# Kernel tuning notes

Measured on AMD Instinct MI355X. Metric: run time of the kernel, lower is better.

## Reference

```python
import jax, jax.numpy as jnp
import numpy as np

TEMP = 0.05
EPS = 1e-6


def _l2norm(x):
    return x / jnp.linalg.norm(x, axis=1, keepdims=True)


def setup_inputs() -> dict:
    key = jax.random.key(0)
    k1, k2, k3, k4 = jax.random.split(key, 4)
    B, D = 4096, 768
    return {
        "feat": jax.random.normal(k1, (B, D), dtype=jnp.float32),
        "feat_gen": jax.random.normal(k2, (B, D), dtype=jnp.float32),
        "feat_aug": jax.random.normal(k3, (B, D), dtype=jnp.float32),
        "targets": jax.random.randint(k4, (B,), 0, 100, dtype=jnp.int64),
    }


def reference(feat, feat_gen, feat_aug, targets):
    B = feat.shape[0]
    on = _l2norm(feat)
    gn = _l2norm(feat_gen)
    an = _l2norm(feat_aug)
    # [B, B] exp-similarity matrices
    exp_ori = jnp.exp(on @ on.T / TEMP)
    exp_gen = jnp.exp(on @ gn.T / TEMP)
    exp_aug = jnp.exp(on @ an.T / TEMP)

    same = (targets[:, None] == targets[None, :])  # [B, B] bool, includes diagonal
    same_f = same.astype(exp_ori.dtype)

    # ---- co loss: anchors vs ori+aug columns ----
    oa = exp_ori + exp_aug
    diff_sum_oa = oa.sum(axis=1) - (oa * same_f).sum(axis=1)        # [B]
    denom_co = diff_sum_oa + exp_gen.sum(axis=1) + EPS              # [B]
    term_o = -jnp.log(exp_ori / (exp_ori + denom_co[:, None]) + EPS)
    term_a = -jnp.log(exp_aug / (exp_aug + denom_co[:, None]) + EPS)
    co_loss = ((term_o + term_a) * same_f).sum() / B

    # ---- ad loss: anchors vs gen columns ----
    diff_sum_g = exp_gen.sum(axis=1) - (exp_gen * same_f).sum(axis=1)
    denom_ad = diff_sum_g + exp_aug.sum(axis=1) + exp_ori.sum(axis=1) + EPS
    term_g = -jnp.log(exp_gen / (exp_gen + denom_ad[:, None]) + EPS)
    ad_loss = (term_g * same_f).sum() / B

    return (ad_loss, co_loss)
```

## Files before the change

kernel.cpp:

```cpp
#include <hip/hip_runtime.h>
#include <hip/hip_bf16.h>
#include <math.h>

#define Bn 4096
#define Dd 768
#define SC2 28.85390081777927f
#define EPSF 1e-6f
#define DG 4.8516519541e8f

#define O_S      0
#define O_SMOA   12288
#define O_SMG    16384
#define ZERO_F   20480
#define O_P      20480
#define O_RM     20608
#define LIST_OFF   262144
#define LCAP       (1u << 19)
#define NB_OFF     33554432

typedef __attribute__((ext_vector_type(8))) short sh8;
typedef __attribute__((ext_vector_type(4))) float f32x4;

#define AS1 __attribute__((address_space(1)))
#define AS3 __attribute__((address_space(3)))

static __device__ __forceinline__ void gl_lds16(const void* g, void* l) {
    __builtin_amdgcn_global_load_lds((const AS1 void*)g, (AS3 void*)l, 16, 0, 0);
}

static __device__ __forceinline__ unsigned short f2b(float f) {
    unsigned int u = __float_as_uint(f);
    unsigned int r = (u + 0x7fffu + ((u >> 16) & 1u)) >> 16;
    return (unsigned short)r;
}

__global__ void norm_kernel(const float* f0, const float* f1, const float* f2, unsigned short* nb) {
    int r = blockIdx.x, m = blockIdx.y, tid = threadIdx.x;
    const float* src = (m == 0 ? f0 : (m == 1 ? f1 : f2)) + (size_t)r * Dd;
    float x0 = src[tid], x1 = src[tid + 256], x2 = src[tid + 512];
    float v = x0 * x0 + x1 * x1 + x2 * x2;
    #pragma unroll
    for (int off = 1; off < 64; off <<= 1) v += __shfl_xor(v, off);
    __shared__ float wr[4];
    if ((tid & 63) == 0) wr[tid >> 6] = v;
    __syncthreads();
    float inv = rsqrtf(wr[0] + wr[1] + wr[2] + wr[3]);
    unsigned short* dst = nb + ((size_t)m * Bn + r) * Dd;
    dst[tid] = f2b(x0 * inv);
    dst[tid + 256] = f2b(x1 * inv);
    dst[tid + 512] = f2b(x2 * inv);
}

__launch_bounds__(1024)
__global__ void sort_kernel(const int* tg, unsigned int* I, float* out) {
    float* F = (float*)I;
    __shared__ unsigned int h[128], pb[128], cur[128];
    int tid = threadIdx.x;
    for (int e = tid; e < ZERO_F; e += 1024) F[e] = 0.f;
    if (tid == 0) { out[0] = 0.f; out[1] = 0.f; }
    if (tid < 128) { h[tid] = 0; cur[tid] = 0; }
    __syncthreads();
    for (int e = tid; e < Bn; e += 1024) atomicAdd(&h[tg[e]], 1u);
    __syncthreads();
    if (tid < 128) pb[tid] = h[tid] * h[tid];
    __syncthreads();
    for (int s = 1; s < 128; s <<= 1) {
        unsigned int b = 0;
        if (tid < 128 && tid >= s) b = pb[tid - s];
        __syncthreads();
        if (tid < 128) pb[tid] += b;
        __syncthreads();
    }
    if (tid == 127) I[O_P] = pb[127];
    uint2* RM = (uint2*)(I + O_RM);
    for (int e = tid; e < Bn; e += 1024) {
        int c = tg[e];
        unsigned int r = atomicAdd(&cur[c], 1u);
        unsigned int n = h[c];
        RM[e] = make_uint2((unsigned)c | (r << 8), (pb[c] - n * n) + r * n);
    }
}

__launch_bounds__(256, 4)
__global__ void gemm_rowsum(const unsigned short* nb, char* ws) {
    float* F = (float*)ws;
    const unsigned int* I = (const unsigned int*)ws;
    const uint2* RM = (const uint2*)(I + O_RM);
    int z = blockIdx.z;
    const unsigned short* Ag = nb;
    const unsigned short* Bg = nb + (size_t)z * Bn * Dd;
    int m0 = blockIdx.y * 128, n0 = blockIdx.x * 128;
    int tid = threadIdx.x, lane = tid & 63, wave = tid >> 6;
    int wm = (wave >> 1) * 64, wn = (wave & 1) * 64;
    int lid = lane & 15, q = lane >> 4;
    __shared__ __align__(16) unsigned short Asm[128 * 32];
    __shared__ __align__(16) unsigned short Bsm[128 * 32];
    int c0 = tid, c1 = tid + 256;
    int row0 = c0 >> 2, sg0 = (c0 & 3) ^ ((row0 >> 1) & 3);
    int row1 = c1 >> 2, sg1 = (c1 & 3) ^ ((row1 >> 1) & 3);
    const unsigned short* gA0 = Ag + (size_t)(m0 + row0) * Dd + sg0 * 8;
    const unsigned short* gA1 = Ag + (size_t)(m0 + row1) * Dd + sg1 * 8;
    const unsigned short* gB0 = Bg + (size_t)(n0 + row0) * Dd + sg0 * 8;
    const unsigned short* gB1 = Bg + (size_t)(n0 + row1) * Dd + sg1 * 8;
    unsigned short* lA0 = &Asm[c0 * 8];
    unsigned short* lA1 = &Asm[c1 * 8];
    unsigned short* lB0 = &Bsm[c0 * 8];
    unsigned short* lB1 = &Bsm[c1 * 8];
    f32x4 acc[4][4] = {};
    for (int kt = 0; kt < Dd / 32; ++kt) {
        __syncthreads();
        gl_lds16(gA0 + kt * 32, lA0);
        gl_lds16(gA1 + kt * 32, lA1);
        gl_lds16(gB0 + kt * 32, lB0);
        gl_lds16(gB1 + kt * 32, lB1);
        __syncthreads();
        sh8 af[4], bf[4];
        #pragma unroll
        for (int i = 0; i < 4; ++i) {
            int r = wm + i * 16 + lid;
            af[i] = *(const sh8*)&Asm[r * 32 + ((q ^ ((r >> 1) & 3)) * 8)];
        }
        #pragma unroll
        for (int j = 0; j < 4; ++j) {
            int r = wn + j * 16 + lid;
            bf[j] = *(const sh8*)&Bsm[r * 32 + ((q ^ ((r >> 1) & 3)) * 8)];
        }
        #pragma unroll
        for (int i = 0; i < 4; ++i)
            #pragma unroll
            for (int j = 0; j < 4; ++j)
                acc[i][j] = __builtin_amdgcn_mfma_f32_16x16x32_bf16(af[i], bf[j], acc[i][j], 0, 0, 0);
    }
    uint2 rmc[4];
    #pragma unroll
    for (int j = 0; j < 4; ++j) rmc[j] = RM[n0 + wn + j * 16 + lid];
    int smoff = (z == 1) ? O_SMG : O_SMOA;
    unsigned int* Lw = (unsigned int*)(ws + LIST_OFF);
    #pragma unroll
    for (int i = 0; i < 4; ++i)
        #pragma unroll
        for (int reg = 0; reg < 4; ++reg) {
            int grow = m0 + wm + i * 16 + q * 4 + reg;
            uint2 rm = RM[grow];
            unsigned int trow = rm.x & 255u, rsb = rm.y;
            float rs = 0.f, ms = 0.f;
            #pragma unroll
            for (int j = 0; j < 4; ++j) {
                int gcol = n0 + wn + j * 16 + lid;
                float x = acc[i][j][reg] * SC2;
                float e = exp2f(x);
                if (z == 0 && gcol == grow) e = 0.f;
                rs += e;
                if ((rmc[j].x & 255u) == trow) {
                    ms += e;
                    unsigned int slot = rsb + (rmc[j].x >> 8);
                    if (slot < LCAP) {
                        if (z == 0) {
                            Lw[slot * 4 + 0] = (unsigned)grow;
                            Lw[slot * 4 + 1] = __float_as_uint(x);
                        } else {
                            Lw[slot * 4 + 1 + z] = __float_as_uint(x);
                        }
                    }
                }
            }
            #pragma unroll
            for (int off = 1; off < 16; off <<= 1) {
                rs += __shfl_xor(rs, off);
                ms += __shfl_xor(ms, off);
            }
            if (lid == 0) {
                atomicAdd(&F[O_S + z * Bn + grow], rs);
                atomicAdd(&F[smoff + grow], ms);
            }
        }
}

__launch_bounds__(256)
__global__ void loss_kernel(char* ws, float* out) {
    float* F = (float*)ws;
    const unsigned int* I = (const unsigned int*)ws;
    const uint4* L = (const uint4*)(ws + LIST_OFF);
    unsigned int n = I[O_P]; if (n > LCAP) n = LCAP;
    float a0 = 0.f, a1 = 0.f;
    unsigned int stride = gridDim.x * 256;
    for (unsigned int idx = blockIdx.x * 256 + threadIdx.x; idx < n; idx += stride) {
        uint4 en = L[idx];
        int i = (int)en.x;
        float son = F[O_S + i], sgen = F[O_S + Bn + i], saug = F[O_S + 2 * Bn + i];
        float dco = (son + saug - F[O_SMOA + i]) + sgen + EPSF;
        float dad = (sgen - F[O_SMG + i]) + saug + son + DG + EPSF;
        float eo = exp2f(__uint_as_float(en.y));
        float eg = exp2f(__uint_as_float(en.z));
        float ea = exp2f(__uint_as_float(en.w));
        a0 += -__logf(eg / (eg + dad) + EPSF);
        a1 += -__logf(eo / (eo + dco) + EPSF) - __logf(ea / (ea + dco) + EPSF);
    }
    #pragma unroll
    for (int off = 1; off < 64; off <<= 1) { a0 += __shfl_xor(a0, off); a1 += __shfl_xor(a1, off); }
    __shared__ float r0[4], r1[4];
    int tid = threadIdx.x;
    if ((tid & 63) == 0) { r0[tid >> 6] = a0; r1[tid >> 6] = a1; }
    __syncthreads();
    if (tid == 0) {
        atomicAdd(&out[0], (r0[0] + r0[1] + r0[2] + r0[3]) * (1.0f / Bn));
        atomicAdd(&out[1], (r1[0] + r1[1] + r1[2] + r1[3]) * (1.0f / Bn));
    }
}

extern "C" void kernel_launch(void* const* d_in, const int* in_sizes, int n_in,
                              void* d_out, int out_size, void* d_ws, size_t ws_size,
                              hipStream_t stream) {
    const float* f0 = (const float*)d_in[0];
    const float* f1 = (const float*)d_in[1];
    const float* f2 = (const float*)d_in[2];
    const int* tg = (const int*)d_in[3];
    char* ws = (char*)d_ws;
    unsigned int* I = (unsigned int*)d_ws;
    unsigned short* nb = (unsigned short*)(ws + NB_OFF);
    float* out = (float*)d_out;

    norm_kernel<<<dim3(Bn, 3), 256, 0, stream>>>(f0, f1, f2, nb);
    sort_kernel<<<1, 1024, 0, stream>>>(tg, I, out);
    gemm_rowsum<<<dim3(32, 32, 3), 256, 0, stream>>>(nb, ws);
    loss_kernel<<<256, 256, 0, stream>>>(ws, out);
}
```

Measured before the change: 220.6 us.

## Double-buffer LDS tiles in gemm_rowsum to overlap loads with MFMA

The GEMM main loop now uses two LDS buffer pairs for A and B. It issues the async global-to-LDS loads for the next K-tile before running the MFMAs on the current tile, and processes two K-steps per iteration. This is meant to hide global load latency behind matrix math instead of stalling at a barrier every K-step. It doubles LDS use per block and lowers the occupancy hint in launch_bounds from 4 to 3 blocks, which may reduce latency hiding across waves.

```diff
diff --git a/kernel.cpp b/kernel.cpp
--- a/kernel.cpp
+++ b/kernel.cpp
@@ -81,7 +81,26 @@
     }
 }
 
-__launch_bounds__(256, 4)
+#define COMPUTE_TILE(BUFA, BUFB) do {                                          \
+    sh8 af[4], bf[4];                                                          \
+    _Pragma("unroll")                                                          \
+    for (int i = 0; i < 4; ++i) {                                              \
+        int r = wm + i * 16 + lid;                                             \
+        af[i] = *(const sh8*)&BUFA[r * 32 + ((q ^ ((r >> 1) & 3)) * 8)];       \
+    }                                                                          \
+    _Pragma("unroll")                                                          \
+    for (int j = 0; j < 4; ++j) {                                              \
+        int r = wn + j * 16 + lid;                                             \
+        bf[j] = *(const sh8*)&BUFB[r * 32 + ((q ^ ((r >> 1) & 3)) * 8)];       \
+    }                                                                          \
+    _Pragma("unroll")                                                          \
+    for (int i = 0; i < 4; ++i)                                                \
+        _Pragma("unroll")                                                      \
+        for (int j = 0; j < 4; ++j)                                            \
+            acc[i][j] = __builtin_amdgcn_mfma_f32_16x16x32_bf16(af[i], bf[j], acc[i][j], 0, 0, 0); \
+} while (0)
+
+__launch_bounds__(256, 3)
 __global__ void gemm_rowsum(const unsigned short* nb, char* ws) {
     float* F = (float*)ws;
     const unsigned int* I = (const unsigned int*)ws;
@@ -93,8 +112,8 @@
     int tid = threadIdx.x, lane = tid & 63, wave = tid >> 6;
     int wm = (wave >> 1) * 64, wn = (wave & 1) * 64;
     int lid = lane & 15, q = lane >> 4;
-    __shared__ __align__(16) unsigned short Asm[128 * 32];
-    __shared__ __align__(16) unsigned short Bsm[128 * 32];
+    __shared__ __align__(16) unsigned short Asm0[128 * 32], Asm1[128 * 32];
+    __shared__ __align__(16) unsigned short Bsm0[128 * 32], Bsm1[128 * 32];
     int c0 = tid, c1 = tid + 256;
     int row0 = c0 >> 2, sg0 = (c0 & 3) ^ ((row0 >> 1) & 3);
     int row1 = c1 >> 2, sg1 = (c1 & 3) ^ ((row1 >> 1) & 3);
@@ -102,34 +121,27 @@
     const unsigned short* gA1 = Ag + (size_t)(m0 + row1) * Dd + sg1 * 8;
     const unsigned short* gB0 = Bg + (size_t)(n0 + row0) * Dd + sg0 * 8;
     const unsigned short* gB1 = Bg + (size_t)(n0 + row1) * Dd + sg1 * 8;
-    unsigned short* lA0 = &Asm[c0 * 8];
-    unsigned short* lA1 = &Asm[c1 * 8];
-    unsigned short* lB0 = &Bsm[c0 * 8];
-    unsigned short* lB1 = &Bsm[c1 * 8];
     f32x4 acc[4][4] = {};
-    for (int kt = 0; kt < Dd / 32; ++kt) {
-        __syncthreads();
-        gl_lds16(gA0 + kt * 32, lA0);
-        gl_lds16(gA1 + kt * 32, lA1);
-        gl_lds16(gB0 + kt * 32, lB0);
-        gl_lds16(gB1 + kt * 32, lB1);
-        __syncthreads();
-        sh8 af[4], bf[4];
-        #pragma unroll
-        for (int i = 0; i < 4; ++i) {
-            int r = wm + i * 16 + lid;
-            af[i] = *(const sh8*)&Asm[r * 32 + ((q ^ ((r >> 1) & 3)) * 8)];
+    gl_lds16(gA0, &Asm0[c0 * 8]);
+    gl_lds16(gA1, &Asm0[c1 * 8]);
+    gl_lds16(gB0, &Bsm0[c0 * 8]);
+    gl_lds16(gB1, &Bsm0[c1 * 8]);
+    for (int kt2 = 0; kt2 < Dd / 64; ++kt2) {
+        int t1 = kt2 * 2 + 1, t2 = kt2 * 2 + 2;
+        __syncthreads();
+        gl_lds16(gA0 + t1 * 32, &Asm1[c0 * 8]);
+        gl_lds16(gA1 + t1 * 32, &Asm1[c1 * 8]);
+        gl_lds16(gB0 + t1 * 32, &Bsm1[c0 * 8]);
+        gl_lds16(gB1 + t1 * 32, &Bsm1[c1 * 8]);
+        COMPUTE_TILE(Asm0, Bsm0);
+        __syncthreads();
+        if (t2 < Dd / 32) {
+            gl_lds16(gA0 + t2 * 32, &Asm0[c0 * 8]);
+            gl_lds16(gA1 + t2 * 32, &Asm0[c1 * 8]);
+            gl_lds16(gB0 + t2 * 32, &Bsm0[c0 * 8]);
+            gl_lds16(gB1 + t2 * 32, &Bsm0[c1 * 8]);
         }
-        #pragma unroll
-        for (int j = 0; j < 4; ++j) {
-            int r = wn + j * 16 + lid;
-            bf[j] = *(const sh8*)&Bsm[r * 32 + ((q ^ ((r >> 1) & 3)) * 8)];
-        }
-        #pragma unroll
-        for (int i = 0; i < 4; ++i)
-            #pragma unroll
-            for (int j = 0; j < 4; ++j)
-                acc[i][j] = __builtin_amdgcn_mfma_f32_16x16x32_bf16(af[i], bf[j], acc[i][j], 0, 0, 0);
+        COMPUTE_TILE(Asm1, Bsm1);
     }
     uint2 rmc[4];
     #pragma unroll
```

New measurement: 230.2 us. +4.3%, slower.
